# Kernel optimization log

Hardware: AMD Instinct MI355X
Metric: run time of the kernel (lower is better)

The kernel has to match this reference:

```python
import jax, jax.numpy as jnp
import numpy as np

# Daubechies-4 decomposition filters (pywt 'db4', ascending order)
_DB4_DEC_LO = np.array([-0.010597401784997278, 0.032883011666982945,
                        0.030841381835986965, -0.18703481171888114,
                        -0.02798376941698385, 0.6308807679295904,
                        0.7148465705525415, 0.23037781330885523])
_DB4_DEC_HI = np.array([-0.23037781330885523, 0.7148465705525415,
                        -0.6308807679295904, -0.02798376941698385,
                        0.18703481171888114, 0.030841381835986965,
                        -0.032883011666982945, -0.010597401784997278])

J_LEVELS = 3


def setup_inputs() -> dict:
    key = jax.random.key(0)
    x = jax.random.normal(key, (16, 64, 65536), dtype=jnp.float32)
    # prep_filt_afb1d stores the REVERSED filters; conv2d cross-correlation with
    # reversed taps == true convolution with the original wavelet filter.
    h0 = jnp.asarray(_DB4_DEC_LO[::-1].copy(), dtype=jnp.float32)  # (L,)
    h1 = jnp.asarray(_DB4_DEC_HI[::-1].copy(), dtype=jnp.float32)  # (L,)
    return {"x": x, "h0": h0, "h1": h1}


def _afb1d_per(x, h0r, h1r):
    """One periodic analysis level. x: (B, C, N) with N even.
    Mirrors afb1d: roll by -L/2, zero-pad L-1, stride-2 depthwise conv,
    wrap-around slice-add, keep first N/2 samples."""
    B, C, N = x.shape
    L = h0r.shape[0]
    L2 = L // 2
    N2 = N // 2
    xr = jnp.roll(x, -L2, axis=-1)
    xp = jnp.pad(xr, ((0, 0), (0, 0), (L - 1, L - 1)))
    # same filter for every channel -> fold (B, C) into batch, 2 output taps
    k = jnp.stack([h0r, h1r])[:, None, :]  # (2, 1, L)
    y = jax.lax.conv_general_dilated(
        xp.reshape(B * C, 1, N + 2 * (L - 1)), k,
        window_strides=(2,), padding='VALID',
        dimension_numbers=('NCH', 'OIH', 'NCH'))  # (B*C, 2, N2 + L2)
    y = y.at[..., :L2].add(y[..., N2:N2 + L2])[..., :N2]
    y = y.reshape(B, C, 2, N2)
    return y[:, :, 0], y[:, :, 1]  # lo, hi


def reference(x, h0, h1):
    highs = []
    x0 = x
    for _ in range(J_LEVELS):
        x0, x1 = _afb1d_per(x0, h0, h1)
        highs.append(x1)
    return (x0, *highs)
```

## Files before the change

kernel.cpp:

```cpp
#include <hip/hip_runtime.h>


#define N0      65536
#define CHUNK_S 8192
#define NROWS   1024
#define BD      512

#define OFF_LO3 0ul
#define OFF_HI1 8388608ul
#define OFF_HI2 41943040ul
#define OFF_HI3 58720256ul

__global__ __launch_bounds__(BD, 4)
void dwt3_fused(const float* __restrict__ x,
                const float* __restrict__ h0,
                const float* __restrict__ h1,
                float* __restrict__ out) {
    __shared__ __align__(16) float sx[8238];
    __shared__ __align__(16) float slo1[4117];
    __shared__ __align__(16) float slo2[2054];

    const int tid   = threadIdx.x;
    const int bid   = blockIdx.x;
    const int row   = bid >> 3;
    const int chunk = bid & 7;
    const int base  = chunk * CHUNK_S;
    const size_t rowOff = (size_t)row * N0;

    float h0f[8], h1f[8];
#pragma unroll
    for (int t = 0; t < 8; ++t) { h0f[t] = h0[t]; h1f[t] = h1[t]; }

    const float4* x4 = reinterpret_cast<const float4*>(x + rowOff + base);
#pragma unroll
    for (int m = tid; m < CHUNK_S / 4; m += BD) {
        float4 v = x4[m];
        int p = 23 + 4 * m;
        sx[p]   = v.x; sx[p+1] = v.y; sx[p+2] = v.z; sx[p+3] = v.w;
    }
    for (int i = tid; i < 46; i += BD) {
        int g, p;
        if (i < 23) { g = base - 23 + i;           p = i; }
        else        { g = base + CHUNK_S + (i-23); p = CHUNK_S + i; }
        if (g < 0)    g += N0;
        if (g >= N0)  g -= N0;
        sx[p] = x[rowOff + g];
    }
    __syncthreads();

    const float2* sx2 = reinterpret_cast<const float2*>(sx);
    float* hi1 = out + OFF_HI1 + (size_t)row * 32768 + (size_t)chunk * 4096;
    for (int kk = tid; kk < 4116; kk += BD) {
        float2 p0 = sx2[kk], p1 = sx2[kk+1], p2 = sx2[kk+2], p3 = sx2[kk+3];
        float v[8] = {p0.x, p0.y, p1.x, p1.y, p2.x, p2.y, p3.x, p3.y};
        float s0 = 0.f, s1 = 0.f;
#pragma unroll
        for (int t = 0; t < 8; ++t) {
            s0 = fmaf(h0f[t], v[t], s0);
            s1 = fmaf(h1f[t], v[t], s1);
        }
        slo1[kk + 1] = s0;
        unsigned k = (unsigned)(kk - 10);
        if (k < 4096u) hi1[k] = s1;
    }
    __syncthreads();

    const float2* slo1_2 = reinterpret_cast<const float2*>(slo1);
    float* hi2 = out + OFF_HI2 + (size_t)row * 16384 + (size_t)chunk * 2048;
    for (int jj = tid; jj < 2054; jj += BD) {
        float2 q0 = slo1_2[jj+1], q1 = slo1_2[jj+2], q2 = slo1_2[jj+3], q3 = slo1_2[jj+4];
        float v[8] = {q0.x, q0.y, q1.x, q1.y, q2.x, q2.y, q3.x, q3.y};
        float s0 = 0.f, s1 = 0.f;
#pragma unroll
        for (int t = 0; t < 8; ++t) {
            s0 = fmaf(h0f[t], v[t], s0);
            s1 = fmaf(h1f[t], v[t], s1);
        }
        slo2[jj] = s0;
        unsigned j = (unsigned)(jj - 3);
        if (j < 2048u) hi2[j] = s1;
    }
    __syncthreads();

    const float2* slo2_2 = reinterpret_cast<const float2*>(slo2);
    float* lo3 = out + OFF_LO3 + (size_t)row * 8192 + (size_t)chunk * 1024;
    float* hi3 = out + OFF_HI3 + (size_t)row * 8192 + (size_t)chunk * 1024;
    for (int ii = tid; ii < 1024; ii += BD) {
        float2 r0 = slo2_2[ii], r1 = slo2_2[ii+1], r2 = slo2_2[ii+2], r3 = slo2_2[ii+3];
        float v[8] = {r0.x, r0.y, r1.x, r1.y, r2.x, r2.y, r3.x, r3.y};
        float s0 = 0.f, s1 = 0.f;
#pragma unroll
        for (int t = 0; t < 8; ++t) {
            s0 = fmaf(h0f[t], v[t], s0);
            s1 = fmaf(h1f[t], v[t], s1);
        }
        lo3[ii] = s0;
        hi3[ii] = s1;
    }
}

extern "C" void kernel_launch(void* const* d_in, const int* in_sizes, int n_in,
                              void* d_out, int out_size, void* d_ws, size_t ws_size,
                              hipStream_t stream) {
    const float* x  = (const float*)d_in[0];
    const float* h0 = (const float*)d_in[1];
    const float* h1 = (const float*)d_in[2];
    float* out = (float*)d_out;
    (void)in_sizes; (void)n_in; (void)out_size; (void)d_ws; (void)ws_size;

    dim3 grid(NROWS * 8);
    dim3 block(BD);
    dwt3_fused<<<grid, block, 0, stream>>>(x, h0, h1, out);
}
```

Measured before the change: 433.7 us.

## Halve chunk size and compute two adjacent outputs per thread with vector LDS loads

Splits each row into 16 chunks of 4096 samples instead of 8 of 8192, doubling the grid and cutting shared memory per block. Each thread now computes two adjacent lo/hi outputs from one float4+float4+float2 shared-memory read, reusing the overlapping window, and writes level-3 outputs as float2. The aim is fewer LDS loads per output and higher occupancy. The cost is more halo recomputation per chunk and lower thread utilization in the later stages, where only 256 of 512 threads are active in level 3.

```diff
diff --git a/kernel.cpp b/kernel.cpp
--- a/kernel.cpp
+++ b/kernel.cpp
@@ -2,8 +2,7 @@
 
 
 #define N0      65536
-#define CHUNK_S 8192
-#define NROWS   1024
+#define S       4096
 #define BD      512
 
 #define OFF_LO3 0ul
@@ -11,20 +10,37 @@
 #define OFF_HI2 41943040ul
 #define OFF_HI3 58720256ul
 
+#define SX_OFF  25
+#define SX_SZ   4152
+#define SLO1_SZ 2072
+#define SLO2_SZ 1032
+
+#define QUAD(vv, L0, G0, L1, G1)                                     \
+    {                                                                \
+        L0 = 0.f; G0 = 0.f; L1 = 0.f; G1 = 0.f;                      \
+        _Pragma("unroll")                                            \
+        for (int t = 0; t < 8; ++t) {                                \
+            L0 = fmaf(h0f[t], vv[t],     L0);                        \
+            G0 = fmaf(h1f[t], vv[t],     G0);                        \
+            L1 = fmaf(h0f[t], vv[t + 2], L1);                        \
+            G1 = fmaf(h1f[t], vv[t + 2], G1);                        \
+        }                                                            \
+    }
+
 __global__ __launch_bounds__(BD, 4)
 void dwt3_fused(const float* __restrict__ x,
                 const float* __restrict__ h0,
                 const float* __restrict__ h1,
                 float* __restrict__ out) {
-    __shared__ __align__(16) float sx[8238];
-    __shared__ __align__(16) float slo1[4117];
-    __shared__ __align__(16) float slo2[2054];
+    __shared__ __align__(16) float sx[SX_SZ];
+    __shared__ __align__(16) float slo1[SLO1_SZ];
+    __shared__ __align__(16) float slo2[SLO2_SZ];
 
     const int tid   = threadIdx.x;
     const int bid   = blockIdx.x;
-    const int row   = bid >> 3;
-    const int chunk = bid & 7;
-    const int base  = chunk * CHUNK_S;
+    const int row   = bid >> 4;
+    const int chunk = bid & 15;
+    const int base  = chunk * S;
     const size_t rowOff = (size_t)row * N0;
 
     float h0f[8], h1f[8];
@@ -33,69 +49,69 @@
 
     const float4* x4 = reinterpret_cast<const float4*>(x + rowOff + base);
 #pragma unroll
-    for (int m = tid; m < CHUNK_S / 4; m += BD) {
+    for (int m = tid; m < S / 4; m += BD) {
         float4 v = x4[m];
-        int p = 23 + 4 * m;
-        sx[p]   = v.x; sx[p+1] = v.y; sx[p+2] = v.z; sx[p+3] = v.w;
+        int p = SX_OFF + 4 * m;
+        sx[p] = v.x; sx[p+1] = v.y; sx[p+2] = v.z; sx[p+3] = v.w;
     }
-    for (int i = tid; i < 46; i += BD) {
+    if (tid < 56) {
         int g, p;
-        if (i < 23) { g = base - 23 + i;           p = i; }
-        else        { g = base + CHUNK_S + (i-23); p = CHUNK_S + i; }
+        if (tid < 25) { g = base - 25 + tid;       p = tid; }
+        else          { g = base + S + (tid - 25); p = SX_OFF + S + (tid - 25); }
         if (g < 0)    g += N0;
         if (g >= N0)  g -= N0;
         sx[p] = x[rowOff + g];
     }
     __syncthreads();
 
-    const float2* sx2 = reinterpret_cast<const float2*>(sx);
-    float* hi1 = out + OFF_HI1 + (size_t)row * 32768 + (size_t)chunk * 4096;
-    for (int kk = tid; kk < 4116; kk += BD) {
-        float2 p0 = sx2[kk], p1 = sx2[kk+1], p2 = sx2[kk+2], p3 = sx2[kk+3];
-        float v[8] = {p0.x, p0.y, p1.x, p1.y, p2.x, p2.y, p3.x, p3.y};
-        float s0 = 0.f, s1 = 0.f;
-#pragma unroll
-        for (int t = 0; t < 8; ++t) {
-            s0 = fmaf(h0f[t], v[t], s0);
-            s1 = fmaf(h1f[t], v[t], s1);
-        }
-        slo1[kk + 1] = s0;
-        unsigned k = (unsigned)(kk - 10);
-        if (k < 4096u) hi1[k] = s1;
+    float* hi1 = out + OFF_HI1 + (size_t)row * 32768 + (size_t)chunk * 2048;
+    for (int pp = tid; pp < 1035; pp += BD) {
+        const float* sp = sx + 4 * pp + 4;
+        float4 a = *reinterpret_cast<const float4*>(sp);
+        float4 b = *reinterpret_cast<const float4*>(sp + 4);
+        float2 c = *reinterpret_cast<const float2*>(sp + 8);
+        float v[10] = {a.x, a.y, a.z, a.w, b.x, b.y, b.z, b.w, c.x, c.y};
+        float l0, g0, l1, g1;
+        QUAD(v, l0, g0, l1, g1);
+        int kk = 2 * pp;
+        *reinterpret_cast<float2*>(slo1 + kk) = make_float2(l0, l1);
+        unsigned m0 = (unsigned)(kk - 9);
+        unsigned m1 = (unsigned)(kk - 8);
+        if (m0 < 2048u) hi1[m0] = g0;
+        if (m1 < 2048u) hi1[m1] = g1;
     }
     __syncthreads();
 
-    const float2* slo1_2 = reinterpret_cast<const float2*>(slo1);
-    float* hi2 = out + OFF_HI2 + (size_t)row * 16384 + (size_t)chunk * 2048;
-    for (int jj = tid; jj < 2054; jj += BD) {
-        float2 q0 = slo1_2[jj+1], q1 = slo1_2[jj+2], q2 = slo1_2[jj+3], q3 = slo1_2[jj+4];
-        float v[8] = {q0.x, q0.y, q1.x, q1.y, q2.x, q2.y, q3.x, q3.y};
-        float s0 = 0.f, s1 = 0.f;
-#pragma unroll
-        for (int t = 0; t < 8; ++t) {
-            s0 = fmaf(h0f[t], v[t], s0);
-            s1 = fmaf(h1f[t], v[t], s1);
-        }
-        slo2[jj] = s0;
-        unsigned j = (unsigned)(jj - 3);
-        if (j < 2048u) hi2[j] = s1;
+    float* hi2 = out + OFF_HI2 + (size_t)row * 16384 + (size_t)chunk * 1024;
+    for (int qq = tid; qq < 516; qq += BD) {
+        const float* sp = slo1 + 4 * qq;
+        float4 a = *reinterpret_cast<const float4*>(sp);
+        float4 b = *reinterpret_cast<const float4*>(sp + 4);
+        float2 c = *reinterpret_cast<const float2*>(sp + 8);
+        float v[10] = {a.x, a.y, a.z, a.w, b.x, b.y, b.z, b.w, c.x, c.y};
+        float l0, g0, l1, g1;
+        QUAD(v, l0, g0, l1, g1);
+        int jj = 2 * qq;
+        *reinterpret_cast<float2*>(slo2 + jj) = make_float2(l0, l1);
+        unsigned m0 = (unsigned)(jj - 3);
+        unsigned m1 = (unsigned)(jj - 2);
+        if (m0 < 1024u) hi2[m0] = g0;
+        if (m1 < 1024u) hi2[m1] = g1;
     }
     __syncthreads();
 
-    const float2* slo2_2 = reinterpret_cast<const float2*>(slo2);
-    float* lo3 = out + OFF_LO3 + (size_t)row * 8192 + (size_t)chunk * 1024;
-    float* hi3 = out + OFF_HI3 + (size_t)row * 8192 + (size_t)chunk * 1024;
-    for (int ii = tid; ii < 1024; ii += BD) {
-        float2 r0 = slo2_2[ii], r1 = slo2_2[ii+1], r2 = slo2_2[ii+2], r3 = slo2_2[ii+3];
-        float v[8] = {r0.x, r0.y, r1.x, r1.y, r2.x, r2.y, r3.x, r3.y};
-        float s0 = 0.f, s1 = 0.f;
-#pragma unroll
-        for (int t = 0; t < 8; ++t) {
-            s0 = fmaf(h0f[t], v[t], s0);
-            s1 = fmaf(h1f[t], v[t], s1);
-        }
-        lo3[ii] = s0;
-        hi3[ii] = s1;
+    float* lo3 = out + OFF_LO3 + (size_t)row * 8192 + (size_t)chunk * 512;
+    float* hi3 = out + OFF_HI3 + (size_t)row * 8192 + (size_t)chunk * 512;
+    for (int pp = tid; pp < 256; pp += BD) {
+        const float* sp = slo2 + 4 * pp;
+        float4 a = *reinterpret_cast<const float4*>(sp);
+        float4 b = *reinterpret_cast<const float4*>(sp + 4);
+        float2 c = *reinterpret_cast<const float2*>(sp + 8);
+        float v[10] = {a.x, a.y, a.z, a.w, b.x, b.y, b.z, b.w, c.x, c.y};
+        float l0, g0, l1, g1;
+        QUAD(v, l0, g0, l1, g1);
+        *reinterpret_cast<float2*>(lo3 + 2 * pp) = make_float2(l0, l1);
+        *reinterpret_cast<float2*>(hi3 + 2 * pp) = make_float2(g0, g1);
     }
 }
 
@@ -108,7 +124,7 @@
     float* out = (float*)d_out;
     (void)in_sizes; (void)n_in; (void)out_size; (void)d_ws; (void)ws_size;
 
-    dim3 grid(NROWS * 8);
+    dim3 grid(1024 * 16);
     dim3 block(BD);
     dwt3_fused<<<grid, block, 0, stream>>>(x, h0, h1, out);
 }
```

Measured after the change: 429.0 us. Within noise of the previous version (-1.1%).
